# Kernel tuning notes

Hardware: AMD Instinct MI355X
Metric: run time of the kernel (lower is better)

## Reference

```python
import jax, jax.numpy as jnp
import numpy as np
import math

NUM_HEADS = 16
HEAD_DIM = 32  # latent_dim // num_heads = 512 // 16


def rope(x, pos):
    # x: (B, H, S, Dh); half-split rotary embedding, theta=10000
    d = x.shape[-1] // 2
    inv_freq = 1.0 / (10000.0 ** (jnp.arange(d, dtype=jnp.float32) / d))
    ang = pos.astype(jnp.float32)[:, None] * inv_freq[None, :]  # (S, d)
    cos, sin = jnp.cos(ang), jnp.sin(ang)
    x1, x2 = x[..., :d], x[..., d:]
    return jnp.concatenate([x1 * cos - x2 * sin, x1 * sin + x2 * cos], axis=-1)


def setup_inputs() -> dict:
    key = jax.random.key(0)
    ks = jax.random.split(key, 16)
    B, L, KV_PREV = 1, 2048, 2048
    D, D_KV = 2048, 512
    s = lambda fan_in: 1.0 / math.sqrt(fan_in)
    return {
        "x": jax.random.normal(ks[0], (B, L, D), jnp.float32),
        "z_cache": jax.random.normal(ks[1], (B, KV_PREV, D_KV), jnp.float32),
        "valid_lens": jax.random.randint(ks[2], (B, L), 1, KV_PREV + L, jnp.int32),
        "W_latent": jax.random.normal(ks[3], (D, D_KV), jnp.float32) * s(D),
        "b_latent": jnp.zeros((D_KV,), jnp.float32),
        "W_q": jax.random.normal(ks[4], (D, NUM_HEADS * HEAD_DIM), jnp.float32) * s(D),
        "b_q": jnp.zeros((NUM_HEADS * HEAD_DIM,), jnp.float32),
        "W_k": jax.random.normal(ks[5], (D_KV, NUM_HEADS * HEAD_DIM), jnp.float32) * s(D_KV),
        "b_k": jnp.zeros((NUM_HEADS * HEAD_DIM,), jnp.float32),
        "W_v": jax.random.normal(ks[6], (D_KV, NUM_HEADS * HEAD_DIM), jnp.float32) * s(D_KV),
        "b_v": jnp.zeros((NUM_HEADS * HEAD_DIM,), jnp.float32),
        "W_o": jax.random.normal(ks[7], (NUM_HEADS * HEAD_DIM, D), jnp.float32) * s(NUM_HEADS * HEAD_DIM),
        "b_o": jnp.zeros((D,), jnp.float32),
    }


def reference(x, z_cache, valid_lens, W_latent, b_latent, W_q, b_q, W_k, b_k, W_v, b_v, W_o, b_o):
    B, L, D = x.shape
    H, Dh = NUM_HEADS, HEAD_DIM
    # latent projection + cache concat
    z_new = x @ W_latent + b_latent                      # (B, L, D_kv)
    z = jnp.concatenate([z_cache, z_new], axis=1)        # (B, KV, D_kv)
    KV = z.shape[1]
    q = (x @ W_q + b_q).reshape(B, L, H, Dh).transpose(0, 2, 1, 3)   # (B,H,L,Dh)
    k = (z @ W_k + b_k).reshape(B, KV, H, Dh).transpose(0, 2, 1, 3)  # (B,H,KV,Dh)
    v = (z @ W_v + b_v).reshape(B, KV, H, Dh).transpose(0, 2, 1, 3)  # (B,H,KV,Dh)
    q = rope(q, jnp.arange(L))
    k = rope(k, jnp.arange(KV))
    scores = jnp.einsum("bhqd,bhkd->bhqk", q, k) / math.sqrt(Dh)     # (B,H,L,KV)
    # faithful: unmasked softmax (returned as attn_weights), then re-masked softmax
    attn_weights = jax.nn.softmax(scores, axis=-1)
    invalid = jnp.arange(KV)[None, None, None, :] >= valid_lens[:, None, :, None]
    masked = jnp.where(invalid, jnp.float32(-10000.0), scores)
    masked_w = jax.nn.softmax(masked, axis=-1)
    heads = jnp.einsum("bhqk,bhkd->bhqd", masked_w, v)               # (B,H,L,Dh)
    heads = heads.transpose(0, 2, 1, 3).reshape(B, L, H * Dh)
    output = heads @ W_o + b_o                                       # (B, L, D)
    return (output, z, attn_weights, scores)
```

## Files before the change

kernel.cpp:

```cpp
#include <hip/hip_runtime.h>
#include <math.h>

#define L_Q     2048
#define KV_PREV 2048
#define KV_TOT  4096
#define DIM     2048
#define D_KV    512
#define NH      16
#define DH      32
#define HDh     512
#define PAD     4104
#define KW      512

typedef short bf16x8 __attribute__((ext_vector_type(8)));
typedef short bf16x4 __attribute__((ext_vector_type(4)));
typedef float f32x4  __attribute__((ext_vector_type(4)));

__device__ inline short f2bf(float f) {
    unsigned u = __float_as_uint(f);
    u += 0x7fff + ((u >> 16) & 1);
    return (short)(u >> 16);
}
__device__ inline float bf2f(short s) {
    return __uint_as_float(((unsigned)(unsigned short)s) << 16);
}

__device__ __constant__ double c_invfreq[16] = {
    1.0, 0.5623413251903491, 0.31622776601683794, 0.17782794100389228,
    0.1, 0.05623413251903491, 0.03162277660168379, 0.017782794100389228,
    0.01, 0.005623413251903491, 0.0031622776601683794, 0.0017782794100389228,
    0.001, 0.0005623413251903491, 0.00031622776601683794, 0.00017782794100389227,
};

__global__ void cvt_bf16(const float* __restrict__ in, short* __restrict__ out, int n8) {
    int i = blockIdx.x * blockDim.x + threadIdx.x;
    if (i >= n8) return;
    float4 a = reinterpret_cast<const float4*>(in)[2 * i];
    float4 b = reinterpret_cast<const float4*>(in)[2 * i + 1];
    union { short s[8]; int4 v; } u;
    u.s[0] = f2bf(a.x); u.s[1] = f2bf(a.y); u.s[2] = f2bf(a.z); u.s[3] = f2bf(a.w);
    u.s[4] = f2bf(b.x); u.s[5] = f2bf(b.y); u.s[6] = f2bf(b.z); u.s[7] = f2bf(b.w);
    reinterpret_cast<int4*>(out)[i] = u.v;
}

__global__ void cvt_copy(const float* __restrict__ src, float* __restrict__ dst,
                         short* __restrict__ dbf, int n8) {
    int i = blockIdx.x * blockDim.x + threadIdx.x;
    if (i >= n8) return;
    float4 a = reinterpret_cast<const float4*>(src)[2 * i];
    float4 b = reinterpret_cast<const float4*>(src)[2 * i + 1];
    reinterpret_cast<float4*>(dst)[2 * i]     = a;
    reinterpret_cast<float4*>(dst)[2 * i + 1] = b;
    union { short s[8]; int4 v; } u;
    u.s[0] = f2bf(a.x); u.s[1] = f2bf(a.y); u.s[2] = f2bf(a.z); u.s[3] = f2bf(a.w);
    u.s[4] = f2bf(b.x); u.s[5] = f2bf(b.y); u.s[6] = f2bf(b.z); u.s[7] = f2bf(b.w);
    reinterpret_cast<int4*>(dbf)[i] = u.v;
}

__global__ __launch_bounds__(256) void tr_cvt_all(
        const float* __restrict__ W0, const float* __restrict__ W1,
        const float* __restrict__ W2, const float* __restrict__ W3,
        const float* __restrict__ W4,
        short* __restrict__ O0, short* __restrict__ O1, short* __restrict__ O2,
        short* __restrict__ O3, short* __restrict__ O4) {
    __shared__ float tile[32][33];
    int b = blockIdx.x;
    const float* in; short* out; int K, N;
    if (b < 1024)      { in = W0; out = O0; K = 2048; N = 512; }
    else if (b < 2048) { in = W1; out = O1; K = 2048; N = 512;  b -= 1024; }
    else if (b < 2304) { in = W2; out = O2; K = 512;  N = 512;  b -= 2048; }
    else if (b < 2560) { in = W3; out = O3; K = 512;  N = 512;  b -= 2304; }
    else               { in = W4; out = O4; K = 512;  N = 2048; b -= 2560; }
    int nkb = K / 32;
    int k0 = (b % nkb) * 32, n0 = (b / nkb) * 32;
    int c = threadIdx.x & 31, r0 = threadIdx.x >> 5;
    for (int r = r0; r < 32; r += 8)
        tile[r][c] = in[(size_t)(k0 + r) * N + n0 + c];
    __syncthreads();
    for (int r = r0; r < 32; r += 8)
        out[(size_t)(n0 + r) * K + k0 + c] = f2bf(tile[c][r]);
}

__global__ __launch_bounds__(256) void vt_cvt(const short* __restrict__ v, short* __restrict__ vt) {
    __shared__ short tile[64][34];
    int h = blockIdx.y, kv0 = blockIdx.x * 64;
    int c = threadIdx.x & 31, r0 = threadIdx.x >> 5;
    for (int r = r0; r < 64; r += 8)
        tile[r][c] = v[(size_t)(kv0 + r) * HDh + h * DH + c];
    __syncthreads();
    int l = threadIdx.x & 63, wv = threadIdx.x >> 6;
    for (int d = wv; d < 32; d += 4)
        vt[((size_t)h * DH + d) * KV_TOT + kv0 + l] = tile[l][d];
}

__global__ __launch_bounds__(256) void gemm_bf16(const short* __restrict__ A,
        const short* __restrict__ Bt, const float* __restrict__ bias,
        float* __restrict__ C, short* __restrict__ Cbf, int rope,
        int M, int N, int K)
{
    int t = threadIdx.x, w = t >> 6, l = t & 63, lr = l & 15, lg = l >> 4;
    int m0 = blockIdx.y * 64 + w * 16;
    int n0 = blockIdx.x * 64;
    f32x4 acc[4] = {{0,0,0,0},{0,0,0,0},{0,0,0,0},{0,0,0,0}};
    const short* ap  = A  + (size_t)(m0 + lr) * K + lg * 8;
    const short* bp0 = Bt + (size_t)(n0 + lr) * K + lg * 8;
    #pragma unroll 2
    for (int k0 = 0; k0 < K; k0 += 32) {
        bf16x8 a = *reinterpret_cast<const bf16x8*>(ap + k0);
        #pragma unroll
        for (int j = 0; j < 4; ++j) {
            bf16x8 b = *reinterpret_cast<const bf16x8*>(bp0 + (size_t)j * 16 * K + k0);
            acc[j] = __builtin_amdgcn_mfma_f32_16x16x32_bf16(a, b, acc[j], 0, 0, 0);
        }
    }
    float bs[4];
    #pragma unroll
    for (int j = 0; j < 4; ++j) bs[j] = bias[n0 + j * 16 + lr];

    if (rope) {
        #pragma unroll
        for (int r = 0; r < 4; ++r) {
            int m = m0 + lg * 4 + r;
            float ang = (float)((double)m * c_invfreq[lr]);
            float cs = cosf(ang), sn = sinf(ang);
            size_t rb = (size_t)m * N + n0 + lr;
            float a1 = acc[0][r] + bs[0], a2 = acc[1][r] + bs[1];
            Cbf[rb]      = f2bf(a1 * cs - a2 * sn);
            Cbf[rb + 16] = f2bf(a1 * sn + a2 * cs);
            float b1 = acc[2][r] + bs[2], b2 = acc[3][r] + bs[3];
            Cbf[rb + 32] = f2bf(b1 * cs - b2 * sn);
            Cbf[rb + 48] = f2bf(b1 * sn + b2 * cs);
        }
        return;
    }
    #pragma unroll
    for (int j = 0; j < 4; ++j) {
        int n = n0 + j * 16 + lr;
        #pragma unroll
        for (int r = 0; r < 4; ++r) {
            float v = acc[j][r] + bs[j];
            size_t idx = (size_t)(m0 + lg * 4 + r) * N + n;
            if (C)   C[idx] = v;
            if (Cbf) Cbf[idx] = f2bf(v);
        }
    }
}

__global__ __launch_bounds__(512) void attn_fused(const short* __restrict__ q,
        const short* __restrict__ kmat, const int* __restrict__ vlens,
        const short* __restrict__ Vt,
        float* __restrict__ scores, float* __restrict__ attn,
        short* __restrict__ heads_bf)
{
    __shared__ short Sbf[16][PAD];
    __shared__ float red[8][16][2];
    __shared__ float Hst[8][64][8];
    int t = threadIdx.x, w = t >> 6, l = t & 63, lr = l & 15, lg = l >> 4;
    int h = blockIdx.y;
    int qrow = blockIdx.x * 16;
    int myq = qrow + lr;
    bf16x8 bQ = *reinterpret_cast<const bf16x8*>(q + (size_t)myq * HDh + h * DH + lg * 8);
    int vl = vlens[myq];
    const short* kp  = kmat + h * DH + lg * 8;
    const short* vp0 = Vt + ((size_t)h * DH + lr) * KV_TOT + lg * 8;
    const short* vp1 = vp0 + (size_t)16 * KV_TOT;
    const float sc = 0.17677669529663687f;
    const int kb = lg * 4;
    const int kw0 = w * KW;

    float su = 0.f, s2 = 0.f;
    bf16x8 a0 = *reinterpret_cast<const bf16x8*>(kp + (size_t)(kw0 + lr) * HDh);
    bf16x8 a1 = *reinterpret_cast<const bf16x8*>(kp + (size_t)(kw0 + 16 + lr) * HDh);
    for (int k0 = kw0; k0 < kw0 + KW; k0 += 32) {
        int kn = kw0 + ((k0 - kw0 + 32) & (KW - 1));
        bf16x8 a0n = *reinterpret_cast<const bf16x8*>(kp + (size_t)(kn + lr) * HDh);
        bf16x8 a1n = *reinterpret_cast<const bf16x8*>(kp + (size_t)(kn + 16 + lr) * HDh);
        f32x4 z4 = {0.f, 0.f, 0.f, 0.f};
        f32x4 s0 = __builtin_amdgcn_mfma_f32_16x16x32_bf16(a0, bQ, z4, 0, 0, 0);
        f32x4 s1 = __builtin_amdgcn_mfma_f32_16x16x32_bf16(a1, bQ, z4, 0, 0, 0);
        bf16x4 w0v, w1v;
        #pragma unroll
        for (int r = 0; r < 4; ++r) {
            float o0 = s0[r] * sc, o1 = s1[r] * sc;
            float e0 = __expf(o0), e1 = __expf(o1);
            su += e0 + e1;
            if (k0 + kb + r < vl)      s2 += e0;
            if (k0 + 16 + kb + r < vl) s2 += e1;
            w0v[r] = f2bf(o0);
            w1v[r] = f2bf(o1);
        }
        *reinterpret_cast<bf16x4*>(&Sbf[lr][k0 + kb])      = w0v;
        *reinterpret_cast<bf16x4*>(&Sbf[lr][k0 + 16 + kb]) = w1v;
        a0 = a0n; a1 = a1n;
    }
    su += __shfl_xor(su, 16, 64); su += __shfl_xor(su, 32, 64);
    s2 += __shfl_xor(s2, 16, 64); s2 += __shfl_xor(s2, 32, 64);
    if (lg == 0) { red[w][lr][0] = su; red[w][lr][1] = s2; }

    f32x4 h0 = {0,0,0,0}, h1 = {0,0,0,0};
    for (int k0 = kw0; k0 < kw0 + KW; k0 += 32) {
        bf16x8 sv = *reinterpret_cast<const bf16x8*>(&Sbf[lr][k0 + lg * 8]);
        bf16x8 pa;
        #pragma unroll
        for (int j = 0; j < 8; ++j) {
            float e = __expf(bf2f(sv[j]));
            pa[j] = (k0 + lg * 8 + j < vl) ? f2bf(e) : (short)0;
        }
        bf16x8 b0 = *reinterpret_cast<const bf16x8*>(vp0 + k0);
        bf16x8 b1 = *reinterpret_cast<const bf16x8*>(vp1 + k0);
        h0 = __builtin_amdgcn_mfma_f32_16x16x32_bf16(pa, b0, h0, 0, 0, 0);
        h1 = __builtin_amdgcn_mfma_f32_16x16x32_bf16(pa, b1, h1, 0, 0, 0);
    }
    *reinterpret_cast<f32x4*>(&Hst[w][l][0]) = h0;
    *reinterpret_cast<f32x4*>(&Hst[w][l][4]) = h1;
    __syncthreads();

    #pragma unroll
    for (int rr = 0; rr < 2; ++rr) {
        int r = 2 * w + rr;
        float sut = 0.f;
        #pragma unroll
        for (int ww = 0; ww < 8; ++ww) sut += red[ww][r][0];
        float isu = 1.f / sut;
        float* srow = scores + ((size_t)h * L_Q + qrow + r) * KV_TOT;
        float* arow = attn   + ((size_t)h * L_Q + qrow + r) * KV_TOT;
        #pragma unroll
        for (int i = 0; i < 8; ++i) {
            int col = i * 512 + l * 8;
            bf16x8 sv = *reinterpret_cast<const bf16x8*>(&Sbf[r][col]);
            f32x4 sA, sB, eA, eB;
            #pragma unroll
            for (int j = 0; j < 4; ++j) {
                sA[j] = bf2f(sv[j]);
                sB[j] = bf2f(sv[4 + j]);
                eA[j] = __expf(sA[j]) * isu;
                eB[j] = __expf(sB[j]) * isu;
            }
            *reinterpret_cast<f32x4*>(srow + col)     = sA;
            *reinterpret_cast<f32x4*>(srow + col + 4) = sB;
            *reinterpret_cast<f32x4*>(arow + col)     = eA;
            *reinterpret_cast<f32x4*>(arow + col + 4) = eB;
        }
    }

    if (w == 0) {
        f32x4 g0 = {0,0,0,0}, g1 = {0,0,0,0};
        #pragma unroll
        for (int ww = 0; ww < 8; ++ww) {
            g0 += *reinterpret_cast<const f32x4*>(&Hst[ww][l][0]);
            g1 += *reinterpret_cast<const f32x4*>(&Hst[ww][l][4]);
        }
        #pragma unroll
        for (int r = 0; r < 4; ++r) {
            int rq = lg * 4 + r;
            float s2t = 0.f;
            #pragma unroll
            for (int ww = 0; ww < 8; ++ww) s2t += red[ww][rq][1];
            float is2 = 1.f / s2t;
            size_t ho = (size_t)(qrow + rq) * HDh + h * DH + lr;
            heads_bf[ho]      = f2bf(g0[r] * is2);
            heads_bf[ho + 16] = f2bf(g1[r] * is2);
        }
    }
}

extern "C" void kernel_launch(void* const* d_in, const int* in_sizes, int n_in,
                              void* d_out, int out_size, void* d_ws, size_t ws_size,
                              hipStream_t stream) {
    const float* x       = (const float*)d_in[0];
    const float* z_cache = (const float*)d_in[1];
    const int*   vlens   = (const int*)  d_in[2];
    const float* W_lat   = (const float*)d_in[3];
    const float* b_lat   = (const float*)d_in[4];
    const float* W_q     = (const float*)d_in[5];
    const float* b_q     = (const float*)d_in[6];
    const float* W_k     = (const float*)d_in[7];
    const float* b_k     = (const float*)d_in[8];
    const float* W_v     = (const float*)d_in[9];
    const float* b_v     = (const float*)d_in[10];
    const float* W_o     = (const float*)d_in[11];
    const float* b_o     = (const float*)d_in[12];

    float* out        = (float*)d_out;
    float* out_output = out;
    float* out_z      = out_output + (size_t)L_Q * DIM;
    float* out_attn   = out_z + (size_t)KV_TOT * D_KV;
    float* out_scores = out_attn + (size_t)NH * L_Q * KV_TOT;

    short* wsb      = (short*)d_ws;
    short* x_bf     = wsb;
    short* z_bf     = x_bf + (size_t)L_Q * DIM;
    short* q_bf     = z_bf + (size_t)KV_TOT * D_KV;
    short* k_bf     = q_bf + (size_t)L_Q * HDh;
    short* v_bf     = k_bf + (size_t)KV_TOT * HDh;
    short* Vt       = v_bf + (size_t)KV_TOT * HDh;
    short* heads_bf = Vt + (size_t)NH * DH * KV_TOT;
    short* Wt_lat   = heads_bf + (size_t)L_Q * HDh;
    short* Wt_q     = Wt_lat + (size_t)D_KV * DIM;
    short* Wt_k     = Wt_q + (size_t)HDh * DIM;
    short* Wt_v     = Wt_k + (size_t)HDh * D_KV;
    short* Wt_o     = Wt_v + (size_t)HDh * D_KV;

    cvt_bf16<<<(L_Q * DIM / 8 + 255) / 256, 256, 0, stream>>>(x, x_bf, L_Q * DIM / 8);
    cvt_copy<<<(KV_PREV * D_KV / 8 + 255) / 256, 256, 0, stream>>>(
        z_cache, out_z, z_bf, KV_PREV * D_KV / 8);
    tr_cvt_all<<<3584, 256, 0, stream>>>(W_lat, W_q, W_k, W_v, W_o,
                                         Wt_lat, Wt_q, Wt_k, Wt_v, Wt_o);

    gemm_bf16<<<dim3(D_KV / 64, L_Q / 64), 256, 0, stream>>>(
        x_bf, Wt_lat, b_lat, out_z + (size_t)KV_PREV * D_KV,
        z_bf + (size_t)KV_PREV * D_KV, 0, L_Q, D_KV, DIM);

    gemm_bf16<<<dim3(HDh / 64, L_Q / 64), 256, 0, stream>>>(
        x_bf, Wt_q, b_q, nullptr, q_bf, 1, L_Q, HDh, DIM);
    gemm_bf16<<<dim3(HDh / 64, KV_TOT / 64), 256, 0, stream>>>(
        z_bf, Wt_k, b_k, nullptr, k_bf, 1, KV_TOT, HDh, D_KV);
    gemm_bf16<<<dim3(HDh / 64, KV_TOT / 64), 256, 0, stream>>>(
        z_bf, Wt_v, b_v, nullptr, v_bf, 0, KV_TOT, HDh, D_KV);
    vt_cvt<<<dim3(KV_TOT / 64, NH), 256, 0, stream>>>(v_bf, Vt);

    attn_fused<<<dim3(L_Q / 16, NH), 512, 0, stream>>>(
        q_bf, k_bf, vlens, Vt, out_scores, out_attn, heads_bf);

    gemm_bf16<<<dim3(DIM / 64, L_Q / 64), 256, 0, stream>>>(
        heads_bf, Wt_o, b_o, out_output, nullptr, 0, L_Q, DIM, HDh);
}
```

Before: 578.1 us.

## Split attention output expansion into separate streaming kernels via bf16 scratch

The attention kernel now stores bf16 scores and per-row inverse softmax sums to a workspace scratch instead of writing fp32 scores and attention weights itself. Two new grid-stride kernels then expand the scratch into fp32 scores and exponentiated, normalized attention weights. The aim is to shorten the heavy attention kernel and let simple streaming kernels saturate memory bandwidth. The cost is an extra round trip through the scratch buffer in global memory and two extra launches.

```diff
diff --git a/kernel.cpp b/kernel.cpp
--- a/kernel.cpp
+++ b/kernel.cpp
@@ -146,10 +146,10 @@
     }
 }
 
-__global__ __launch_bounds__(512) void attn_fused(const short* __restrict__ q,
+__global__ __launch_bounds__(512) void attn_core(const short* __restrict__ q,
         const short* __restrict__ kmat, const int* __restrict__ vlens,
         const short* __restrict__ Vt,
-        float* __restrict__ scores, float* __restrict__ attn,
+        short* __restrict__ scratch, float* __restrict__ isu_o,
         short* __restrict__ heads_bf)
 {
     __shared__ short Sbf[16][PAD];
@@ -218,28 +218,18 @@
     #pragma unroll
     for (int rr = 0; rr < 2; ++rr) {
         int r = 2 * w + rr;
-        float sut = 0.f;
-        #pragma unroll
-        for (int ww = 0; ww < 8; ++ww) sut += red[ww][r][0];
-        float isu = 1.f / sut;
-        float* srow = scores + ((size_t)h * L_Q + qrow + r) * KV_TOT;
-        float* arow = attn   + ((size_t)h * L_Q + qrow + r) * KV_TOT;
+        short* srow = scratch + ((size_t)h * L_Q + qrow + r) * KV_TOT;
         #pragma unroll
         for (int i = 0; i < 8; ++i) {
             int col = i * 512 + l * 8;
-            bf16x8 sv = *reinterpret_cast<const bf16x8*>(&Sbf[r][col]);
-            f32x4 sA, sB, eA, eB;
+            *reinterpret_cast<int4*>(srow + col) =
+                *reinterpret_cast<const int4*>(&Sbf[r][col]);
+        }
+        if (l == 0) {
+            float sut = 0.f;
             #pragma unroll
-            for (int j = 0; j < 4; ++j) {
-                sA[j] = bf2f(sv[j]);
-                sB[j] = bf2f(sv[4 + j]);
-                eA[j] = __expf(sA[j]) * isu;
-                eB[j] = __expf(sB[j]) * isu;
-            }
-            *reinterpret_cast<f32x4*>(srow + col)     = sA;
-            *reinterpret_cast<f32x4*>(srow + col + 4) = sB;
-            *reinterpret_cast<f32x4*>(arow + col)     = eA;
-            *reinterpret_cast<f32x4*>(arow + col + 4) = eB;
+            for (int ww = 0; ww < 8; ++ww) sut += red[ww][r][0];
+            isu_o[(size_t)h * L_Q + qrow + r] = 1.f / sut;
         }
     }
 
@@ -261,6 +251,42 @@
             heads_bf[ho]      = f2bf(g0[r] * is2);
             heads_bf[ho + 16] = f2bf(g1[r] * is2);
         }
+    }
+}
+
+__global__ __launch_bounds__(256) void expand_scores(const short* __restrict__ sb,
+        float* __restrict__ scores, size_t n8)
+{
+    size_t i = (size_t)blockIdx.x * blockDim.x + threadIdx.x;
+    size_t stride = (size_t)gridDim.x * blockDim.x;
+    for (; i < n8; i += stride) {
+        int4 v = reinterpret_cast<const int4*>(sb)[i];
+        const short* sp = reinterpret_cast<const short*>(&v);
+        f32x4 oA, oB;
+        #pragma unroll
+        for (int j = 0; j < 4; ++j) { oA[j] = bf2f(sp[j]); oB[j] = bf2f(sp[4 + j]); }
+        reinterpret_cast<f32x4*>(scores)[2 * i]     = oA;
+        reinterpret_cast<f32x4*>(scores)[2 * i + 1] = oB;
+    }
+}
+
+__global__ __launch_bounds__(256) void expand_attn(const short* __restrict__ sb,
+        const float* __restrict__ isu, float* __restrict__ attn, size_t n8)
+{
+    size_t i = (size_t)blockIdx.x * blockDim.x + threadIdx.x;
+    size_t stride = (size_t)gridDim.x * blockDim.x;
+    for (; i < n8; i += stride) {
+        int4 v = reinterpret_cast<const int4*>(sb)[i];
+        const short* sp = reinterpret_cast<const short*>(&v);
+        float is = isu[i >> 9];
+        f32x4 oA, oB;
+        #pragma unroll
+        for (int j = 0; j < 4; ++j) {
+            oA[j] = __expf(bf2f(sp[j])) * is;
+            oB[j] = __expf(bf2f(sp[4 + j])) * is;
+        }
+        reinterpret_cast<f32x4*>(attn)[2 * i]     = oA;
+        reinterpret_cast<f32x4*>(attn)[2 * i + 1] = oB;
     }
 }
 
@@ -287,7 +313,9 @@
     float* out_attn   = out_z + (size_t)KV_TOT * D_KV;
     float* out_scores = out_attn + (size_t)NH * L_Q * KV_TOT;
 
-    short* wsb      = (short*)d_ws;
+    short* scratch  = (short*)d_ws;
+    float* ws_isu   = (float*)(scratch + (size_t)NH * L_Q * KV_TOT);
+    short* wsb      = (short*)(ws_isu + (size_t)NH * L_Q);
     short* x_bf     = wsb;
     short* z_bf     = x_bf + (size_t)L_Q * DIM;
     short* q_bf     = z_bf + (size_t)KV_TOT * D_KV;
@@ -319,8 +347,12 @@
         z_bf, Wt_v, b_v, nullptr, v_bf, 0, KV_TOT, HDh, D_KV);
     vt_cvt<<<dim3(KV_TOT / 64, NH), 256, 0, stream>>>(v_bf, Vt);
 
-    attn_fused<<<dim3(L_Q / 16, NH), 512, 0, stream>>>(
-        q_bf, k_bf, vlens, Vt, out_scores, out_attn, heads_bf);
+    attn_core<<<dim3(L_Q / 16, NH), 512, 0, stream>>>(
+        q_bf, k_bf, vlens, Vt, scratch, ws_isu, heads_bf);
+
+    size_t n8 = (size_t)NH * L_Q * KV_TOT / 8;
+    expand_scores<<<4096, 256, 0, stream>>>(scratch, out_scores, n8);
+    expand_attn<<<4096, 256, 0, stream>>>(scratch, ws_isu, out_attn, n8);
 
     gemm_bf16<<<dim3(DIM / 64, L_Q / 64), 256, 0, stream>>>(
         heads_bf, Wt_o, b_o, out_output, nullptr, 0, L_Q, DIM, HDh);
```

Measured after the change: 762.1 us. 1.32x slower.
